# Performance work log

Measured on AMD Instinct MI355X. Metric: run time of the kernel, lower is better.

## Reference

```python
import jax, jax.numpy as jnp
import numpy as np

B, L, D, OUT, EXP = 4, 4096, 128, 55, 2
D2 = 2 * D

def _ln(x, g, b):
    m = jnp.mean(x, axis=-1, keepdims=True)
    v = jnp.mean((x - m) ** 2, axis=-1, keepdims=True)
    return (x - m) / jnp.sqrt(v + 1e-5) * g + b

def setup_inputs() -> dict:
    key = jax.random.key(0)
    ks = iter(jax.random.split(key, 32))
    w = lambda shape: jax.random.normal(next(ks), shape, jnp.float32) * 0.02
    inp = {
        'x1': jax.random.normal(next(ks), (B, L, D), jnp.float32),
        'x2': jax.random.normal(next(ks), (B, L, D), jnp.float32),
        'ln1_g': jnp.ones((D,)), 'ln1_b': jnp.zeros((D,)),
        'ln2_g': jnp.ones((D,)), 'ln2_b': jnp.zeros((D,)),
        'Wq': w((D, D)), 'bq': jnp.zeros((D,)),
        'Wv1': w((D, D)), 'bv1': jnp.zeros((D,)),
        'Wk': w((D, D)), 'bk': jnp.zeros((D,)),
        'Wv2': w((D, D)), 'bv2': jnp.zeros((D,)),
        'Wp1': w((D, D)), 'bp1': jnp.zeros((D,)),
        'Wp2': w((D, D)), 'bp2': jnp.zeros((D,)),
        'lnf_g': jnp.ones((D2,)), 'lnf_b': jnp.zeros((D2,)),
        'Wf1': w((D2, EXP * D2)), 'bf1': jnp.zeros((EXP * D2,)),
        'Wf2': w((EXP * D2, D2)), 'bf2': jnp.zeros((D2,)),
        'ln3_g': jnp.ones((D2,)), 'ln3_b': jnp.zeros((D2,)),
        'Wo': w((D2, OUT)), 'bo': jnp.zeros((OUT,)),
    }
    return inp

def reference(x1, x2, ln1_g, ln1_b, ln2_g, ln2_b, Wq, bq, Wv1, bv1, Wk, bk,
              Wv2, bv2, Wp1, bp1, Wp2, bp2, lnf_g, lnf_b, Wf1, bf1, Wf2, bf2,
              ln3_g, ln3_b, Wo, bo):
    res1, res2 = x1, x2
    x1n = _ln(x1, ln1_g, ln1_b)
    x2n = _ln(x2, ln2_g, ln2_b)
    q1 = x1n @ Wq + bq        # [B,L,D]
    v1 = x1n @ Wv1 + bv1
    k2 = x2n @ Wk + bk
    v2 = x2n @ Wv2 + bv2
    # faithful to torch: energy = einsum('bqd,bkd->bqk', keys2, queries1)
    energy = jnp.einsum('bqd,bkd->bqk', k2, q1)
    att = jax.nn.softmax(energy / jnp.sqrt(jnp.float32(D)), axis=-1)  # [B,L,L]
    out1 = jnp.einsum('bal,blv->bav', att, v1) @ Wp1 + bp1
    out2 = jnp.einsum('bal,blv->bav', att, v2) @ Wp2 + bp2
    y1 = out1 + res1
    y2 = out2 + res2
    x = jnp.concatenate([y1, y2], axis=-1)  # [B,L,2D]
    res = x
    h = _ln(x, lnf_g, lnf_b)
    h = jax.nn.gelu(h @ Wf1 + bf1, approximate=False) @ Wf2 + bf2
    x = _ln(h + res, ln3_g, ln3_b)
    return x @ Wo + bo  # [B,L,OUT]
```

## Files before the change

### kernel.cpp

```cpp
#include <hip/hip_runtime.h>
#include <hip/hip_fp16.h>

typedef _Float16 half8 __attribute__((ext_vector_type(8)));
typedef _Float16 half4 __attribute__((ext_vector_type(4)));
typedef float f32x4 __attribute__((ext_vector_type(4)));
typedef float f32x16 __attribute__((ext_vector_type(16)));
typedef int  i32x8 __attribute__((ext_vector_type(8)));
typedef long lng2 __attribute__((ext_vector_type(2)));

#define B_   4
#define L_   4096
#define D_   128
#define M_   (B_*L_)
#define D2_  256
#define H_   512
#define OUT_ 55

__device__ __forceinline__ f32x4 mfma16(half8 a, half8 b, f32x4 c) {
    return __builtin_amdgcn_mfma_f32_16x16x32_f16(a, b, c, 0, 0, 0);
}
__device__ __forceinline__ f32x16 mfma_mx32(i32x8 a, i32x8 b, f32x16 c) {
    return __builtin_amdgcn_mfma_scale_f32_32x32x64_f8f6f4(a, b, c, 0, 0, 0, 127, 0, 127);
}
__device__ __forceinline__ int pk4(float a, float b, float c, float d) {
    int t = __builtin_amdgcn_cvt_pk_fp8_f32(a, b, 0, false);
    return __builtin_amdgcn_cvt_pk_fp8_f32(c, d, t, true);
}
__device__ __forceinline__ float fexp2(float x) { return __builtin_amdgcn_exp2f(x); }

#define KSCL (0.08838834764831845f * 1.4426950408889634f)

#define WQ_OFF   0
#define WV1_OFF  16384
#define WK_OFF   32768
#define WV2_OFF  49152
#define WP1_OFF  65536
#define WP2_OFF  81920
#define WF1_OFF  98304
#define WF2_OFF  229376
#define WO_OFF   360448


__global__ void prep_kernel(const float* Wq, const float* Wv1, const float* Wk,
                            const float* Wv2, const float* Wp1, const float* Wp2,
                            const float* Wf1, const float* Wf2, const float* Wo,
                            _Float16* wsw, float* rowsum) {
    int id = blockIdx.y;
    int t  = blockIdx.x * 256 + threadIdx.x;
    if (id == 9) {
        if (t < 4096) ((f32x4*)rowsum)[t] = f32x4{0.f, 0.f, 0.f, 0.f};
        return;
    }
    const float* src = nullptr; int K = 0, N = 0, Npad = 0, off = 0;
    switch (id) {
        case 0: src = Wq;  K = 128; N = 128; Npad = 128; off = WQ_OFF;  break;
        case 1: src = Wv1; K = 128; N = 128; Npad = 128; off = WV1_OFF; break;
        case 2: src = Wk;  K = 128; N = 128; Npad = 128; off = WK_OFF;  break;
        case 3: src = Wv2; K = 128; N = 128; Npad = 128; off = WV2_OFF; break;
        case 4: src = Wp1; K = 128; N = 128; Npad = 128; off = WP1_OFF; break;
        case 5: src = Wp2; K = 128; N = 128; Npad = 128; off = WP2_OFF; break;
        case 6: src = Wf1; K = 256; N = 512; Npad = 512; off = WF1_OFF; break;
        case 7: src = Wf2; K = 512; N = 256; Npad = 256; off = WF2_OFF; break;
        case 8: src = Wo;  K = 256; N = 55;  Npad = 64;  off = WO_OFF;  break;
        default: return;
    }
    int total = K * Npad;
    if (t >= total) return;
    int k = t / Npad, n = t % Npad;
    float v = (n < N) ? src[k * N + n] : 0.f;
    int s = k >> 5, c = n >> 4, ln = n & 15;
    int q, j;
    if (id == 4 || id == 5) { q = (k >> 2) & 3; j = (k & 3) + (((k >> 4) & 1) << 2); }
    else                    { q = (k >> 3) & 3; j = k & 7; }
    int nc = Npad >> 4;
    wsw[off + ((size_t)((s * nc + c) * 64 + q * 16 + ln)) * 8 + j] = (_Float16)v;
}


__global__ __launch_bounds__(256) void proj_kernel(const float* x1, const float* x2,
        const _Float16* wsw,
        const float* ln1_g, const float* ln1_b, const float* ln2_g, const float* ln2_b,
        const float* bq, const float* bv1, const float* bk, const float* bv2,
        _Float16* q1, _Float16* k2, unsigned char* vsw8) {
    int g2 = blockIdx.y;
    const float* X  = g2 ? x2 : x1;
    const float* lg = g2 ? ln2_g : ln1_g;
    const float* lb = g2 ? ln2_b : ln1_b;
    int wave = threadIdx.x >> 6, lane = threadIdx.x & 63;
    int quad = lane >> 4, ln = lane & 15;
    int mbase = blockIdx.x * 64 + wave * 16;
    int lt = mbase >> 4;

    const float* xr = X + (size_t)(mbase + ln) * D_;
    float xv[4][8];
    float sum = 0.f, sq = 0.f;
    #pragma unroll
    for (int s = 0; s < 4; s++) {
        f32x4 v0 = *(const f32x4*)(xr + s * 32 + quad * 8);
        f32x4 v1 = *(const f32x4*)(xr + s * 32 + quad * 8 + 4);
        #pragma unroll
        for (int j = 0; j < 4; j++) {
            xv[s][j]     = v0[j];
            xv[s][j + 4] = v1[j];
            sum += v0[j] + v1[j];
            sq  += v0[j] * v0[j] + v1[j] * v1[j];
        }
    }
    sum += __shfl_xor(sum, 16); sum += __shfl_xor(sum, 32);
    sq  += __shfl_xor(sq, 16);  sq  += __shfl_xor(sq, 32);
    float mean = sum * (1.f / 128.f);
    float var  = sq * (1.f / 128.f) - mean * mean;
    float inv  = rsqrtf(var + 1e-5f);
    half8 a[4];
    #pragma unroll
    for (int s = 0; s < 4; s++) {
        f32x4 g0 = *(const f32x4*)(lg + s * 32 + quad * 8);
        f32x4 g1 = *(const f32x4*)(lg + s * 32 + quad * 8 + 4);
        f32x4 b0 = *(const f32x4*)(lb + s * 32 + quad * 8);
        f32x4 b1 = *(const f32x4*)(lb + s * 32 + quad * 8 + 4);
        #pragma unroll
        for (int j = 0; j < 4; j++) {
            a[s][j]     = (_Float16)((xv[s][j] - mean) * inv * g0[j] + b0[j]);
            a[s][j + 4] = (_Float16)((xv[s][j + 4] - mean) * inv * g1[j] + b1[j]);
        }
    }

    {
        const _Float16* Bw = wsw + (g2 ? WK_OFF : WQ_OFF);
        const float* bias = g2 ? bk : bq;
        float scl = g2 ? KSCL : 1.f;
        _Float16* out = g2 ? k2 : q1;
        f32x4 acc[8];
        #pragma unroll
        for (int c = 0; c < 8; c++) acc[c] = f32x4{0.f, 0.f, 0.f, 0.f};
        half8 Wc[4], Wn[4];
        #pragma unroll
        for (int s = 0; s < 4; s++)
            Wc[s] = *(const half8*)(Bw + ((size_t)((s * 8 + 0) * 64 + lane)) * 8);
        #pragma unroll
        for (int c = 0; c < 8; c++) {
            int cn = (c < 7) ? c + 1 : 7;
            #pragma unroll
            for (int s = 0; s < 4; s++)
                Wn[s] = *(const half8*)(Bw + ((size_t)((s * 8 + cn) * 64 + lane)) * 8);
            #pragma unroll
            for (int s = 0; s < 4; s++)
                acc[c] = mfma16(a[s], Wc[s], acc[c]);
            #pragma unroll
            for (int s = 0; s < 4; s++) Wc[s] = Wn[s];
        }
        #pragma unroll
        for (int c = 0; c < 8; c++) {
            int n = c * 16 + ln;
            float bv = bias[n];
            #pragma unroll
            for (int r = 0; r < 4; r++) {
                int s_o = c >> 1, q_o = ((c & 1) << 1) | (ln >> 3), j = ln & 7;
                out[((size_t)((lt * 4 + s_o) * 64 + q_o * 16 + (quad * 4 + r))) * 8 + j]
                    = (_Float16)((acc[c][r] + bv) * scl);
            }
        }
    }

    {
        const _Float16* Bw = wsw + (g2 ? WV2_OFF : WV1_OFF);
        const float* bias = g2 ? bv2 : bv1;
        int cbase = g2 ? 8 : 0;
        f32x4 acc[8];
        #pragma unroll
        for (int c = 0; c < 8; c++) acc[c] = f32x4{0.f, 0.f, 0.f, 0.f};
        half8 Wc[4], Wn[4];
        #pragma unroll
        for (int s = 0; s < 4; s++)
            Wc[s] = *(const half8*)(Bw + ((size_t)((s * 8 + 0) * 64 + lane)) * 8);
        #pragma unroll
        for (int c = 0; c < 8; c++) {
            int cn = (c < 7) ? c + 1 : 7;
            #pragma unroll
            for (int s = 0; s < 4; s++)
                Wn[s] = *(const half8*)(Bw + ((size_t)((s * 8 + cn) * 64 + lane)) * 8);
            #pragma unroll
            for (int s = 0; s < 4; s++)
                acc[c] = mfma16(a[s], Wc[s], acc[c]);
            #pragma unroll
            for (int s = 0; s < 4; s++) Wc[s] = Wn[s];
        }
        int b = mbase >> 12;
        int k64 = (mbase & (L_ - 1)) >> 6;
        int gg = quad >> 1, jh = quad & 1;
        unsigned char* Vb = vsw8 + (size_t)b * (1u << 20);
        #pragma unroll
        for (int c = 0; c < 8; c++) {
            int n = c * 16 + ln;
            float bv = bias[n];
            int pk = pk4(acc[c][0] + bv, acc[c][1] + bv, acc[c][2] + bv, acc[c][3] + bv);
            int v32 = (cbase + c) >> 1;
            int lane32 = ((c & 1) << 4) + ln + 32 * gg;
            *(int*)(Vb + ((size_t)((k64 * 8 + v32) * 64 + lane32)) * 32 + 16 * jh + 4 * wave) = pk;
        }
    }
}

__global__ __launch_bounds__(256) void score_kernel(
        const _Float16* __restrict__ q1sw, const _Float16* __restrict__ k2sw,
        unsigned char* __restrict__ pmat8, float* __restrict__ rowsum) {
    int w = threadIdx.x >> 6, lane = threadIdx.x & 63;
    int quad = lane >> 4, ln = lane & 15;
    int b = blockIdx.z;
    int kL0 = blockIdx.y * 128 + (w & 1) * 64;
    int mL0 = blockIdx.x * 128 + (w >> 1) * 64;
    int ltk = ((b << 12) + kL0) >> 4;
    int ltm = ((b << 12) + mL0) >> 4;

    f32x4 acc[4][4];
    #pragma unroll
    for (int i = 0; i < 4; i++)
        #pragma unroll
        for (int j = 0; j < 4; j++) acc[i][j] = f32x4{0.f, 0.f, 0.f, 0.f};

    #pragma unroll
    for (int s = 0; s < 4; s++) {
        half8 a[4], bq[4];
        #pragma unroll
        for (int i = 0; i < 4; i++)
            a[i] = *(const half8*)(q1sw + ((size_t)(((ltk + i) * 4 + s) * 64 + lane)) * 8);
        #pragma unroll
        for (int j = 0; j < 4; j++)
            bq[j] = *(const half8*)(k2sw + ((size_t)(((ltm + j) * 4 + s) * 64 + lane)) * 8);
        #pragma unroll
        for (int i = 0; i < 4; i++)
            #pragma unroll
            for (int j = 0; j < 4; j++)
                acc[i][j] = mfma16(a[i], bq[j], acc[i][j]);
    }

    unsigned char* Pb = pmat8 + (size_t)b * (16u << 20);
    int k64 = kL0 >> 6;
    int gg = quad >> 1, jh = quad & 1;
    #pragma unroll
    for (int j = 0; j < 4; j++) {
        int4 d;
        float csum = 0.f;
        #pragma unroll
        for (int i = 0; i < 4; i++) {
            float p0 = fexp2(acc[i][j][0]);
            float p1 = fexp2(acc[i][j][1]);
            float p2 = fexp2(acc[i][j][2]);
            float p3 = fexp2(acc[i][j][3]);
            csum += (p0 + p1) + (p2 + p3);
            ((int*)&d)[i] = pk4(p0, p1, p2, p3);
        }
        csum += __shfl_xor(csum, 16);
        csum += __shfl_xor(csum, 32);
        if (lane < 16)
            atomicAdd(&rowsum[(b << 12) + mL0 + j * 16 + ln], csum);
        int att32 = (mL0 >> 5) + (j >> 1);
        int a32 = ((j & 1) << 4) + ln;
        *(int4*)(Pb + ((size_t)((att32 * 64 + k64) * 64 + a32 + 32 * gg)) * 32 + 16 * jh) = d;
    }
}

__global__ __launch_bounds__(512) void pv_kernel(
        const unsigned char* __restrict__ pmat8, const unsigned char* __restrict__ vsw8,
        const float* __restrict__ rowsum,
        _Float16* __restrict__ att1, _Float16* __restrict__ att2) {
    __shared__ f32x4 part[4][2][4][64];
    int w = threadIdx.x >> 6, lane = threadIdx.x & 63;
    int wc = w & 3, kh = w >> 2;
    int rowG0 = blockIdx.x * 32;
    int b = rowG0 >> 12;
    int att32 = (rowG0 & (L_ - 1)) >> 5;
    const unsigned char* Pb = pmat8 + (size_t)b * (16u << 20);
    const unsigned char* Vb = vsw8 + (size_t)b * (1u << 20);

    const unsigned char* Vbase = Vb + (size_t)(wc * 2) * 2048 + (size_t)lane * 32;
    const unsigned char* Pbase = Pb + (size_t)att32 * 131072 + (size_t)lane * 32;
    int sp0 = kh * 32;

    f32x16 acc0, acc1;
    #pragma unroll
    for (int i = 0; i < 16; i++) { acc0[i] = 0.f; acc1[i] = 0.f; }

    #define PVLOAD(dA, dB, dP, sp) do {                                       \
        dA = *(const i32x8*)(Vbase + (size_t)(sp) * 16384);                   \
        dB = *(const i32x8*)(Vbase + (size_t)(sp) * 16384 + 2048);            \
        dP = *(const i32x8*)(Pbase + (size_t)(sp) * 2048);                    \
    } while (0)

    i32x8 a0, b0, p0, a1, b1, p1, na, nb, np;
    PVLOAD(a0, b0, p0, sp0);
    PVLOAD(a1, b1, p1, sp0 + 1);
    for (int ii = 0; ii < 32; ii += 2) {
        int s2 = sp0 + ((ii + 2 < 32) ? ii + 2 : 31);
        int s3 = sp0 + ((ii + 3 < 32) ? ii + 3 : 31);
        PVLOAD(na, nb, np, s2);
        acc0 = mfma_mx32(a0, p0, acc0);
        acc1 = mfma_mx32(b0, p0, acc1);
        a0 = na; b0 = nb; p0 = np;
        PVLOAD(na, nb, np, s3);
        acc0 = mfma_mx32(a1, p1, acc0);
        acc1 = mfma_mx32(b1, p1, acc1);
        a1 = na; b1 = nb; p1 = np;
    }
    #undef PVLOAD

    if (kh == 1) {
        #pragma unroll
        for (int q = 0; q < 4; q++) {
            part[wc][0][q][lane] = f32x4{acc0[q * 4 + 0], acc0[q * 4 + 1],
                                         acc0[q * 4 + 2], acc0[q * 4 + 3]};
            part[wc][1][q][lane] = f32x4{acc1[q * 4 + 0], acc1[q * 4 + 1],
                                         acc1[q * 4 + 2], acc1[q * 4 + 3]};
        }
    }
    __syncthreads();
    if (kh == 0) {
        int aglob = rowG0 + (lane & 31);
        float inv = 1.f / rowsum[aglob];
        int g = lane >> 5;
        int lt = aglob >> 4, lnr = lane & 15;
        #pragma unroll
        for (int t = 0; t < 2; t++) {
            int v32 = wc * 2 + t;
            _Float16* att = (v32 >= 4) ? att2 : att1;
            int s = v32 & 3;
            #pragma unroll
            for (int q = 0; q < 4; q++) {
                f32x4 pp = part[wc][t][q][lane];
                half4 hv;
                #pragma unroll
                for (int rr = 0; rr < 4; rr++) {
                    float v = ((t == 0) ? acc0[q * 4 + rr] : acc1[q * 4 + rr]) + pp[rr];
                    hv[rr] = (_Float16)(v * inv);
                }
                *(half4*)(att + ((size_t)((lt * 4 + s) * 64 + q * 16 + lnr)) * 8 + 4 * g) = hv;
            }
        }
    }
}

__global__ __launch_bounds__(256) void attn_out_kernel(const _Float16* att1, const _Float16* att2,
        const _Float16* wsw, const float* bp1, const float* bp2,
        const float* x1, const float* x2, const float* lnf_g, const float* lnf_b,
        _Float16* res, _Float16* xn) {
    __shared__ float sst[2][16][2][2];
    int w = threadIdx.x >> 6, lane = threadIdx.x & 63;
    int quad = lane >> 4, ln = lane & 15;
    int rt = w & 1, st = w >> 1;
    int mbase = blockIdx.x * 32 + rt * 16;
    int lt = mbase >> 4;
    const _Float16* att = st ? att2 : att1;
    const _Float16* Wp = wsw + (st ? WP2_OFF : WP1_OFF);
    const float* bp = st ? bp2 : bp1;
    const float* xres = st ? x2 : x1;

    half8 a[4];
    #pragma unroll
    for (int s = 0; s < 4; s++)
        a[s] = *(const half8*)(att + ((size_t)((lt * 4 + s) * 64 + lane)) * 8);

    f32x4 y[8];
    #pragma unroll
    for (int c = 0; c < 8; c++) y[c] = f32x4{0,0,0,0};

    half8 Wc[4], Wn[4];
    #pragma unroll
    for (int s = 0; s < 4; s++)
        Wc[s] = *(const half8*)(Wp + ((size_t)((s * 8 + 0) * 64 + lane)) * 8);
    #pragma unroll
    for (int c = 0; c < 8; c++) {
        int cn = (c < 7) ? c + 1 : 7;
        #pragma unroll
        for (int s = 0; s < 4; s++)
            Wn[s] = *(const half8*)(Wp + ((size_t)((s * 8 + cn) * 64 + lane)) * 8);
        #pragma unroll
        for (int s = 0; s < 4; s++)
            y[c] = mfma16(a[s], Wc[s], y[c]);
        #pragma unroll
        for (int s = 0; s < 4; s++) Wc[s] = Wn[s];
    }

    float psum[4] = {0,0,0,0}, psq[4] = {0,0,0,0};
    #pragma unroll
    for (int c = 0; c < 8; c++) {
        int n = c * 16 + ln;
        float bv = bp[n];
        #pragma unroll
        for (int r = 0; r < 4; r++) {
            int m = mbase + quad * 4 + r;
            float v = y[c][r] + bv + xres[(size_t)m * D_ + n];
            y[c][r] = v; psum[r] += v; psq[r] += v * v;
        }
    }
    #pragma unroll
    for (int off = 1; off < 16; off <<= 1)
        #pragma unroll
        for (int r = 0; r < 4; r++) { psum[r] += __shfl_xor(psum[r], off); psq[r] += __shfl_xor(psq[r], off); }
    if (ln == 0)
        #pragma unroll
        for (int r = 0; r < 4; r++) {
            sst[rt][quad * 4 + r][st][0] = psum[r];
            sst[rt][quad * 4 + r][st][1] = psq[r];
        }
    __syncthreads();
    #pragma unroll
    for (int r = 0; r < 4; r++) {
        float su = sst[rt][quad * 4 + r][0][0] + sst[rt][quad * 4 + r][1][0];
        float sq = sst[rt][quad * 4 + r][0][1] + sst[rt][quad * 4 + r][1][1];
        float mean = su * (1.f / 256.f);
        float var = sq * (1.f / 256.f) - mean * mean;
        float inv = rsqrtf(var + 1e-5f);
        int m = mbase + quad * 4 + r;
        int lt_m = m >> 4;
        #pragma unroll
        for (int c = 0; c < 8; c++) {
            int colg = st * 128 + c * 16 + ln;
            res[(size_t)m * D2_ + colg] = (_Float16)y[c][r];
            float yn = (y[c][r] - mean) * inv * lnf_g[colg] + lnf_b[colg];
            int s_x = colg >> 5, q_x = (colg >> 3) & 3, j = colg & 7;
            xn[((size_t)((lt_m * 8 + s_x) * 64 + q_x * 16 + (m & 15))) * 8 + j] = (_Float16)yn;
        }
    }
}

__global__ __launch_bounds__(256) void ffn1_kernel(const _Float16* xn, const _Float16* wsw,
        const float* bf1, _Float16* h) {
    int wave = threadIdx.x >> 6, lane = threadIdx.x & 63;
    int quad = lane >> 4, ln = lane & 15;
    int mbase = blockIdx.x * 64 + wave * 16;
    int lt = mbase >> 4;
    int nt = blockIdx.y;
    const _Float16* W = wsw + WF1_OFF;

    half8 a[8];
    #pragma unroll
    for (int s = 0; s < 8; s++)
        a[s] = *(const half8*)(xn + ((size_t)((lt * 8 + s) * 64 + lane)) * 8);

    f32x4 acc[8];
    #pragma unroll
    for (int c = 0; c < 8; c++) acc[c] = f32x4{0,0,0,0};

    half8 Wc[8], Wn[8];
    #pragma unroll
    for (int s = 0; s < 8; s++)
        Wc[s] = *(const half8*)(W + ((size_t)((s * 32 + nt * 8) * 64 + lane)) * 8);
    #pragma unroll
    for (int c = 0; c < 8; c++) {
        int cn = (c < 7) ? c + 1 : 7;
        #pragma unroll
        for (int s = 0; s < 8; s++)
            Wn[s] = *(const half8*)(W + ((size_t)((s * 32 + nt * 8 + cn) * 64 + lane)) * 8);
        #pragma unroll
        for (int s = 0; s < 8; s++)
            acc[c] = mfma16(a[s], Wc[s], acc[c]);
        #pragma unroll
        for (int s = 0; s < 8; s++) Wc[s] = Wn[s];
    }
    #pragma unroll
    for (int c = 0; c < 8; c++) {
        int n = nt * 128 + c * 16 + ln;
        float bv = bf1[n];
        int s_h = n >> 5, q_h = (n >> 3) & 3, j = n & 7;
        #pragma unroll
        for (int r = 0; r < 4; r++) {
            float v = acc[c][r] + bv;
            float u = 0.7978845608f * (v + 0.044715f * v * v * v);
            float e = fexp2(-2.8853900818f * u);
            float ge = v * __builtin_amdgcn_rcpf(1.f + e);
            h[((size_t)((lt * 16 + s_h) * 64 + q_h * 16 + (quad * 4 + r))) * 8 + j] = (_Float16)ge;
        }
    }
}

__global__ __launch_bounds__(256) void ffn2_out_kernel(const _Float16* h, const _Float16* wsw,
        const float* bf2, const _Float16* res, const float* g3, const float* b3,
        const float* bo, float* out) {
    __shared__ float sst[2][16][2][2];
    __shared__ _Float16 xt[8192];
    __shared__ f32x4 pc[2][4][64];
    int w = threadIdx.x >> 6, lane = threadIdx.x & 63;
    int quad = lane >> 4, ln = lane & 15;
    int rt = w & 1, nh = w >> 1;
    int mb = blockIdx.x * 32 + rt * 16;
    int lt = mb >> 4;
    const _Float16* W = wsw + WF2_OFF;

    f32x4 acc[8];
    #pragma unroll
    for (int c = 0; c < 8; c++) acc[c] = f32x4{0,0,0,0};

    half8 aC, aN;
    half8 Wc[8], Wn[8];
    aC = *(const half8*)(h + ((size_t)((lt * 16 + 0) * 64 + lane)) * 8);
    #pragma unroll
    for (int c = 0; c < 8; c++)
        Wc[c] = *(const half8*)(W + ((size_t)((0 * 16 + nh * 8 + c) * 64 + lane)) * 8);

    #pragma unroll
    for (int s = 0; s < 16; s++) {
        int sn = (s < 15) ? s + 1 : 15;
        aN = *(const half8*)(h + ((size_t)((lt * 16 + sn) * 64 + lane)) * 8);
        #pragma unroll
        for (int c = 0; c < 8; c++)
            Wn[c] = *(const half8*)(W + ((size_t)((sn * 16 + nh * 8 + c) * 64 + lane)) * 8);
        #pragma unroll
        for (int c = 0; c < 8; c++)
            acc[c] = mfma16(aC, Wc[c], acc[c]);
        aC = aN;
        #pragma unroll
        for (int c = 0; c < 8; c++) Wc[c] = Wn[c];
    }

    float y[8][4];
    float psum[4] = {0,0,0,0}, psq[4] = {0,0,0,0};
    #pragma unroll
    for (int c = 0; c < 8; c++) {
        int n = nh * 128 + c * 16 + ln;
        float bv = bf2[n];
        #pragma unroll
        for (int r = 0; r < 4; r++) {
            int m = mb + quad * 4 + r;
            float v = acc[c][r] + bv + (float)res[(size_t)m * D2_ + n];
            y[c][r] = v; psum[r] += v; psq[r] += v * v;
        }
    }
    #pragma unroll
    for (int off = 1; off < 16; off <<= 1)
        #pragma unroll
        for (int r = 0; r < 4; r++) { psum[r] += __shfl_xor(psum[r], off); psq[r] += __shfl_xor(psq[r], off); }
    if (ln == 0)
        #pragma unroll
        for (int r = 0; r < 4; r++) { sst[rt][quad * 4 + r][nh][0] = psum[r]; sst[rt][quad * 4 + r][nh][1] = psq[r]; }
    __syncthreads();
    #pragma unroll
    for (int r = 0; r < 4; r++) {
        float su = sst[rt][quad * 4 + r][0][0] + sst[rt][quad * 4 + r][1][0];
        float sq = sst[rt][quad * 4 + r][0][1] + sst[rt][quad * 4 + r][1][1];
        float mean = su * (1.f / 256.f);
        float var = sq * (1.f / 256.f) - mean * mean;
        float invs = rsqrtf(var + 1e-5f);
        #pragma unroll
        for (int c = 0; c < 8; c++) {
            int n = nh * 128 + c * 16 + ln;
            float yn = (y[c][r] - mean) * invs * g3[n] + b3[n];
            int s_x = n >> 5, q_x = (n >> 3) & 3, j = n & 7;
            xt[((rt * 8 + s_x) * 64 + q_x * 16 + (quad * 4 + r)) * 8 + j] = (_Float16)yn;
        }
    }
    __syncthreads();

    int rt2 = w & 1, kh = w >> 1;
    const _Float16* Wo = wsw + WO_OFF;
    f32x4 oacc[4];
    #pragma unroll
    for (int c = 0; c < 4; c++) oacc[c] = f32x4{0,0,0,0};
    #pragma unroll
    for (int ss = 0; ss < 4; ss++) {
        int s = kh * 4 + ss;
        half8 a = *(const half8*)(xt + ((size_t)((rt2 * 8 + s) * 64 + lane)) * 8);
        #pragma unroll
        for (int c = 0; c < 4; c++)
            oacc[c] = mfma16(a, *(const half8*)(Wo + ((size_t)((s * 4 + c) * 64 + lane)) * 8), oacc[c]);
    }
    if (kh == 1)
        #pragma unroll
        for (int c = 0; c < 4; c++) pc[rt2][c][lane] = oacc[c];
    __syncthreads();
    if (kh == 0) {
        int mb2 = blockIdx.x * 32 + rt2 * 16;
        #pragma unroll
        for (int c = 0; c < 4; c++) {
            f32x4 p = pc[rt2][c][lane];
            int n = c * 16 + ln;
            if (n < OUT_) {
                float bv = bo[n];
                #pragma unroll
                for (int r = 0; r < 4; r++)
                    out[(size_t)(mb2 + quad * 4 + r) * OUT_ + n] = oacc[c][r] + p[r] + bv;
            }
        }
    }
}

extern "C" void kernel_launch(void* const* d_in, const int* in_sizes, int n_in,
                              void* d_out, int out_size, void* d_ws, size_t ws_size,
                              hipStream_t stream) {
    const float* x1    = (const float*)d_in[0];
    const float* x2    = (const float*)d_in[1];
    const float* ln1_g = (const float*)d_in[2];
    const float* ln1_b = (const float*)d_in[3];
    const float* ln2_g = (const float*)d_in[4];
    const float* ln2_b = (const float*)d_in[5];
    const float* Wq    = (const float*)d_in[6];
    const float* bq    = (const float*)d_in[7];
    const float* Wv1   = (const float*)d_in[8];
    const float* bv1   = (const float*)d_in[9];
    const float* Wk    = (const float*)d_in[10];
    const float* bk    = (const float*)d_in[11];
    const float* Wv2   = (const float*)d_in[12];
    const float* bv2   = (const float*)d_in[13];
    const float* Wp1   = (const float*)d_in[14];
    const float* bp1   = (const float*)d_in[15];
    const float* Wp2   = (const float*)d_in[16];
    const float* bp2   = (const float*)d_in[17];
    const float* lnf_g = (const float*)d_in[18];
    const float* lnf_b = (const float*)d_in[19];
    const float* Wf1   = (const float*)d_in[20];
    const float* bf1   = (const float*)d_in[21];
    const float* Wf2   = (const float*)d_in[22];
    const float* bf2   = (const float*)d_in[23];
    const float* ln3_g = (const float*)d_in[24];
    const float* ln3_b = (const float*)d_in[25];
    const float* Wo    = (const float*)d_in[26];
    const float* bo    = (const float*)d_in[27];
    float* out = (float*)d_out;

    char* ws = (char*)d_ws;
    const size_t MB = 1 << 20;
    _Float16* q1sw   = (_Float16*)(ws + 0 * MB);
    _Float16* k2sw   = (_Float16*)(ws + 4 * MB);
    unsigned char* vsw8 = (unsigned char*)(ws + 8 * MB);
    _Float16* att1   = (_Float16*)(ws + 12 * MB);
    _Float16* att2   = (_Float16*)(ws + 16 * MB);
    _Float16* wsw    = (_Float16*)(ws + 28 * MB);
    float*    rowsum = (float*)   (ws + 29 * MB);
    _Float16* res    = (_Float16*)(ws + 30 * MB);
    _Float16* xn     = (_Float16*)(ws + 46 * MB);
    _Float16* h      = (_Float16*)(ws + 54 * MB);
    unsigned char* pmat8 = (unsigned char*)(ws + 78 * MB);

    prep_kernel<<<dim3(512, 10), 256, 0, stream>>>(Wq, Wv1, Wk, Wv2, Wp1, Wp2, Wf1, Wf2, Wo,
                                                   wsw, rowsum);
    proj_kernel<<<dim3(M_ / 64, 2), 256, 0, stream>>>(x1, x2, wsw,
                                                      ln1_g, ln1_b, ln2_g, ln2_b,
                                                      bq, bv1, bk, bv2,
                                                      q1sw, k2sw, vsw8);
    score_kernel<<<dim3(32, 32, 4), 256, 0, stream>>>(q1sw, k2sw, pmat8, rowsum);
    pv_kernel<<<dim3(M_ / 32), 512, 0, stream>>>(pmat8, vsw8, rowsum, att1, att2);
    attn_out_kernel<<<dim3(M_ / 32), 256, 0, stream>>>(att1, att2, wsw, bp1, bp2,
                                                       x1, x2, lnf_g, lnf_b, res, xn);
    ffn1_kernel<<<dim3(M_ / 64, 4), 256, 0, stream>>>(xn, wsw, bf1, h);
    ffn2_out_kernel<<<dim3(M_ / 32), 256, 0, stream>>>(h, wsw, bf2, res, ln3_g, ln3_b, bo, out);
}
```

Measured before the change: 236.0 us.

## Retile PV kernel so each block covers 128 rows and half the V columns

Each block of the P·V kernel now handles 128 attention rows, with one 32-row group per wave pair, and one of two V halves selected by blockIdx.y, instead of 32 rows across all V columns. Each wave loads one P tile and reuses it across four V sub-tiles, and V tiles are shared by the four row-group waves through cache. This is meant to cut redundant loads of the large FP8 probability matrix, since each P element is now read twice per batch instead of four times. In exchange each wave holds twice as many accumulator and prefetch registers, which may lower occupancy, and LDS use doubles.

```diff
diff --git a/kernel.cpp b/kernel.cpp
--- a/kernel.cpp
+++ b/kernel.cpp
@@ -264,78 +264,90 @@
         const unsigned char* __restrict__ pmat8, const unsigned char* __restrict__ vsw8,
         const float* __restrict__ rowsum,
         _Float16* __restrict__ att1, _Float16* __restrict__ att2) {
-    __shared__ f32x4 part[4][2][4][64];
+    __shared__ f32x4 part[4][4][4][64];
     int w = threadIdx.x >> 6, lane = threadIdx.x & 63;
-    int wc = w & 3, kh = w >> 2;
-    int rowG0 = blockIdx.x * 32;
+    int a = w & 3, kh = w >> 2;
+    int vh = blockIdx.y;
+    int rowG0 = blockIdx.x * 128;
     int b = rowG0 >> 12;
-    int att32 = (rowG0 & (L_ - 1)) >> 5;
+    int att32 = ((rowG0 & (L_ - 1)) >> 5) + a;
     const unsigned char* Pb = pmat8 + (size_t)b * (16u << 20);
     const unsigned char* Vb = vsw8 + (size_t)b * (1u << 20);
 
-    const unsigned char* Vbase = Vb + (size_t)(wc * 2) * 2048 + (size_t)lane * 32;
+    const unsigned char* Vbase = Vb + (size_t)(vh * 4) * 2048 + (size_t)lane * 32;
     const unsigned char* Pbase = Pb + (size_t)att32 * 131072 + (size_t)lane * 32;
     int sp0 = kh * 32;
 
-    f32x16 acc0, acc1;
-    #pragma unroll
-    for (int i = 0; i < 16; i++) { acc0[i] = 0.f; acc1[i] = 0.f; }
-
-    #define PVLOAD(dA, dB, dP, sp) do {                                       \
-        dA = *(const i32x8*)(Vbase + (size_t)(sp) * 16384);                   \
-        dB = *(const i32x8*)(Vbase + (size_t)(sp) * 16384 + 2048);            \
-        dP = *(const i32x8*)(Pbase + (size_t)(sp) * 2048);                    \
+    f32x16 acc0, acc1, acc2, acc3;
+    #pragma unroll
+    for (int i = 0; i < 16; i++) { acc0[i] = 0.f; acc1[i] = 0.f; acc2[i] = 0.f; acc3[i] = 0.f; }
+
+    #define PVLOAD(d0, d1, d2, d3, dp, sp) do {                               \
+        const unsigned char* vp_ = Vbase + (size_t)(sp) * 16384;              \
+        d0 = *(const i32x8*)(vp_);                                            \
+        d1 = *(const i32x8*)(vp_ + 2048);                                     \
+        d2 = *(const i32x8*)(vp_ + 4096);                                     \
+        d3 = *(const i32x8*)(vp_ + 6144);                                     \
+        dp = *(const i32x8*)(Pbase + (size_t)(sp) * 2048);                    \
     } while (0)
 
-    i32x8 a0, b0, p0, a1, b1, p1, na, nb, np;
-    PVLOAD(a0, b0, p0, sp0);
-    PVLOAD(a1, b1, p1, sp0 + 1);
+    i32x8 v00, v01, v02, v03, p0, v10, v11, v12, v13, p1, n0, n1, n2, n3, np;
+    PVLOAD(v00, v01, v02, v03, p0, sp0);
+    PVLOAD(v10, v11, v12, v13, p1, sp0 + 1);
     for (int ii = 0; ii < 32; ii += 2) {
-        int s2 = sp0 + ((ii + 2 < 32) ? ii + 2 : 31);
+        int s2 = sp0 + ((ii + 2 < 32) ? ii + 2 : 30);
         int s3 = sp0 + ((ii + 3 < 32) ? ii + 3 : 31);
-        PVLOAD(na, nb, np, s2);
-        acc0 = mfma_mx32(a0, p0, acc0);
-        acc1 = mfma_mx32(b0, p0, acc1);
-        a0 = na; b0 = nb; p0 = np;
-        PVLOAD(na, nb, np, s3);
-        acc0 = mfma_mx32(a1, p1, acc0);
-        acc1 = mfma_mx32(b1, p1, acc1);
-        a1 = na; b1 = nb; p1 = np;
+        PVLOAD(n0, n1, n2, n3, np, s2);
+        acc0 = mfma_mx32(v00, p0, acc0);
+        acc1 = mfma_mx32(v01, p0, acc1);
+        acc2 = mfma_mx32(v02, p0, acc2);
+        acc3 = mfma_mx32(v03, p0, acc3);
+        v00 = n0; v01 = n1; v02 = n2; v03 = n3; p0 = np;
+        PVLOAD(n0, n1, n2, n3, np, s3);
+        acc0 = mfma_mx32(v10, p1, acc0);
+        acc1 = mfma_mx32(v11, p1, acc1);
+        acc2 = mfma_mx32(v12, p1, acc2);
+        acc3 = mfma_mx32(v13, p1, acc3);
+        v10 = n0; v11 = n1; v12 = n2; v13 = n3; p1 = np;
     }
     #undef PVLOAD
 
     if (kh == 1) {
         #pragma unroll
         for (int q = 0; q < 4; q++) {
-            part[wc][0][q][lane] = f32x4{acc0[q * 4 + 0], acc0[q * 4 + 1],
-                                         acc0[q * 4 + 2], acc0[q * 4 + 3]};
-            part[wc][1][q][lane] = f32x4{acc1[q * 4 + 0], acc1[q * 4 + 1],
-                                         acc1[q * 4 + 2], acc1[q * 4 + 3]};
+            part[a][0][q][lane] = f32x4{acc0[q * 4 + 0], acc0[q * 4 + 1],
+                                        acc0[q * 4 + 2], acc0[q * 4 + 3]};
+            part[a][1][q][lane] = f32x4{acc1[q * 4 + 0], acc1[q * 4 + 1],
+                                        acc1[q * 4 + 2], acc1[q * 4 + 3]};
+            part[a][2][q][lane] = f32x4{acc2[q * 4 + 0], acc2[q * 4 + 1],
+                                        acc2[q * 4 + 2], acc2[q * 4 + 3]};
+            part[a][3][q][lane] = f32x4{acc3[q * 4 + 0], acc3[q * 4 + 1],
+                                        acc3[q * 4 + 2], acc3[q * 4 + 3]};
         }
     }
     __syncthreads();
     if (kh == 0) {
-        int aglob = rowG0 + (lane & 31);
+        int aglob = rowG0 + a * 32 + (lane & 31);
         float inv = 1.f / rowsum[aglob];
         int g = lane >> 5;
         int lt = aglob >> 4, lnr = lane & 15;
-        #pragma unroll
-        for (int t = 0; t < 2; t++) {
-            int v32 = wc * 2 + t;
-            _Float16* att = (v32 >= 4) ? att2 : att1;
-            int s = v32 & 3;
-            #pragma unroll
-            for (int q = 0; q < 4; q++) {
-                f32x4 pp = part[wc][t][q][lane];
-                half4 hv;
-                #pragma unroll
-                for (int rr = 0; rr < 4; rr++) {
-                    float v = ((t == 0) ? acc0[q * 4 + rr] : acc1[q * 4 + rr]) + pp[rr];
-                    hv[rr] = (_Float16)(v * inv);
-                }
-                *(half4*)(att + ((size_t)((lt * 4 + s) * 64 + q * 16 + lnr)) * 8 + 4 * g) = hv;
-            }
-        }
+        _Float16* att = vh ? att2 : att1;
+        #define PVSTORE(accT, t) do {                                         \
+            _Pragma("unroll")                                                 \
+            for (int q = 0; q < 4; q++) {                                     \
+                f32x4 pp = part[a][t][q][lane];                               \
+                half4 hv;                                                     \
+                _Pragma("unroll")                                             \
+                for (int rr = 0; rr < 4; rr++)                                \
+                    hv[rr] = (_Float16)((accT[q * 4 + rr] + pp[rr]) * inv);   \
+                *(half4*)(att + ((size_t)((lt * 4 + (t)) * 64 + q * 16 + lnr)) * 8 + 4 * g) = hv; \
+            }                                                                 \
+        } while (0)
+        PVSTORE(acc0, 0);
+        PVSTORE(acc1, 1);
+        PVSTORE(acc2, 2);
+        PVSTORE(acc3, 3);
+        #undef PVSTORE
     }
 }
 
@@ -637,7 +649,7 @@
                                                       bq, bv1, bk, bv2,
                                                       q1sw, k2sw, vsw8);
     score_kernel<<<dim3(32, 32, 4), 256, 0, stream>>>(q1sw, k2sw, pmat8, rowsum);
-    pv_kernel<<<dim3(M_ / 32), 512, 0, stream>>>(pmat8, vsw8, rowsum, att1, att2);
+    pv_kernel<<<dim3(M_ / 128, 2), 512, 0, stream>>>(pmat8, vsw8, rowsum, att1, att2);
     attn_out_kernel<<<dim3(M_ / 32), 256, 0, stream>>>(att1, att2, wsw, bp1, bp2,
                                                        x1, x2, lnf_g, lnf_b, res, xn);
     ffn1_kernel<<<dim3(M_ / 64, 4), 256, 0, stream>>>(xn, wsw, bf1, h);
```

Result: slower. 245.8 us (+4.1%).

## Switch PV stage to 16x16x128 FP8 MFMA and drop LDS split-K reduction

Applied to the files above, without the earlier changes.

The P·V kernel moves from the 32x32x64 scaled FP8 MFMA with a two-way split over the key dimension to the 16x16x128 variant. Each wave now covers a 16-row tile across the full key range, so the shared-memory partial sums and the __syncthreads reduction go away. The P and V producers in the score and projection kernels are relaid out to match the new operand format, and launch bounds request 4 blocks per CU. The trade-off is that each wave runs a longer serial key loop, P loads are repeated across the V-column waves, and the smaller MFMA shape does less work per operand load.

```diff
diff --git a/kernel.cpp b/kernel.cpp
--- a/kernel.cpp
+++ b/kernel.cpp
@@ -4,9 +4,7 @@
 typedef _Float16 half8 __attribute__((ext_vector_type(8)));
 typedef _Float16 half4 __attribute__((ext_vector_type(4)));
 typedef float f32x4 __attribute__((ext_vector_type(4)));
-typedef float f32x16 __attribute__((ext_vector_type(16)));
 typedef int  i32x8 __attribute__((ext_vector_type(8)));
-typedef long lng2 __attribute__((ext_vector_type(2)));
 
 #define B_   4
 #define L_   4096
@@ -19,8 +17,8 @@
 __device__ __forceinline__ f32x4 mfma16(half8 a, half8 b, f32x4 c) {
     return __builtin_amdgcn_mfma_f32_16x16x32_f16(a, b, c, 0, 0, 0);
 }
-__device__ __forceinline__ f32x16 mfma_mx32(i32x8 a, i32x8 b, f32x16 c) {
-    return __builtin_amdgcn_mfma_scale_f32_32x32x64_f8f6f4(a, b, c, 0, 0, 0, 127, 0, 127);
+__device__ __forceinline__ f32x4 mfma_mx16(i32x8 a, i32x8 b, f32x4 c) {
+    return __builtin_amdgcn_mfma_scale_f32_16x16x128_f8f6f4(a, b, c, 0, 0, 0, 127, 0, 127);
 }
 __device__ __forceinline__ int pk4(float a, float b, float c, float d) {
     int t = __builtin_amdgcn_cvt_pk_fp8_f32(a, b, 0, false);
@@ -165,7 +163,6 @@
     {
         const _Float16* Bw = wsw + (g2 ? WV2_OFF : WV1_OFF);
         const float* bias = g2 ? bv2 : bv1;
-        int cbase = g2 ? 8 : 0;
         f32x4 acc[8];
         #pragma unroll
         for (int c = 0; c < 8; c++) acc[c] = f32x4{0.f, 0.f, 0.f, 0.f};
@@ -186,17 +183,17 @@
             for (int s = 0; s < 4; s++) Wc[s] = Wn[s];
         }
         int b = mbase >> 12;
-        int k64 = (mbase & (L_ - 1)) >> 6;
-        int gg = quad >> 1, jh = quad & 1;
+        int k128 = (mbase & (L_ - 1)) >> 7;
+        int h = (mbase >> 6) & 1;
         unsigned char* Vb = vsw8 + (size_t)b * (1u << 20);
         #pragma unroll
         for (int c = 0; c < 8; c++) {
             int n = c * 16 + ln;
             float bv = bias[n];
             int pk = pk4(acc[c][0] + bv, acc[c][1] + bv, acc[c][2] + bv, acc[c][3] + bv);
-            int v32 = (cbase + c) >> 1;
-            int lane32 = ((c & 1) << 4) + ln + 32 * gg;
-            *(int*)(Vb + ((size_t)((k64 * 8 + v32) * 64 + lane32)) * 32 + 16 * jh + 4 * wave) = pk;
+            int v16 = g2 * 8 + c;
+            *(int*)(Vb + ((size_t)((k128 * 16 + v16) * 64 + quad * 16 + ln)) * 32
+                       + 16 * h + 4 * wave) = pk;
         }
     }
 }
@@ -235,8 +232,8 @@
     }
 
     unsigned char* Pb = pmat8 + (size_t)b * (16u << 20);
-    int k64 = kL0 >> 6;
-    int gg = quad >> 1, jh = quad & 1;
+    int k128 = kL0 >> 7;
+    int kh = (kL0 >> 6) & 1;
     #pragma unroll
     for (int j = 0; j < 4; j++) {
         int4 d;
@@ -254,88 +251,74 @@
         csum += __shfl_xor(csum, 32);
         if (lane < 16)
             atomicAdd(&rowsum[(b << 12) + mL0 + j * 16 + ln], csum);
-        int att32 = (mL0 >> 5) + (j >> 1);
-        int a32 = ((j & 1) << 4) + ln;
-        *(int4*)(Pb + ((size_t)((att32 * 64 + k64) * 64 + a32 + 32 * gg)) * 32 + 16 * jh) = d;
-    }
-}
-
-__global__ __launch_bounds__(512) void pv_kernel(
+        int att16 = (mL0 >> 4) + j;
+        *(int4*)(Pb + ((size_t)((att16 * 32 + k128) * 64 + quad * 16 + ln)) * 32
+                    + 16 * kh) = d;
+    }
+}
+
+__global__ __launch_bounds__(512, 4) void pv_kernel(
         const unsigned char* __restrict__ pmat8, const unsigned char* __restrict__ vsw8,
         const float* __restrict__ rowsum,
         _Float16* __restrict__ att1, _Float16* __restrict__ att2) {
-    __shared__ f32x4 part[4][2][4][64];
     int w = threadIdx.x >> 6, lane = threadIdx.x & 63;
-    int wc = w & 3, kh = w >> 2;
+    int rt = w & 1, vq = w >> 1;
     int rowG0 = blockIdx.x * 32;
     int b = rowG0 >> 12;
-    int att32 = (rowG0 & (L_ - 1)) >> 5;
+    int att16 = ((rowG0 & (L_ - 1)) >> 4) + rt;
     const unsigned char* Pb = pmat8 + (size_t)b * (16u << 20);
     const unsigned char* Vb = vsw8 + (size_t)b * (1u << 20);
-
-    const unsigned char* Vbase = Vb + (size_t)(wc * 2) * 2048 + (size_t)lane * 32;
-    const unsigned char* Pbase = Pb + (size_t)att32 * 131072 + (size_t)lane * 32;
-    int sp0 = kh * 32;
-
-    f32x16 acc0, acc1;
-    #pragma unroll
-    for (int i = 0; i < 16; i++) { acc0[i] = 0.f; acc1[i] = 0.f; }
-
-    #define PVLOAD(dA, dB, dP, sp) do {                                       \
-        dA = *(const i32x8*)(Vbase + (size_t)(sp) * 16384);                   \
-        dB = *(const i32x8*)(Vbase + (size_t)(sp) * 16384 + 2048);            \
-        dP = *(const i32x8*)(Pbase + (size_t)(sp) * 2048);                    \
+    const unsigned char* Pbase = Pb + (size_t)att16 * 65536 + (size_t)lane * 32;
+    const unsigned char* Vbase = Vb + (size_t)(vq * 4) * 2048 + (size_t)lane * 32;
+
+    f32x4 acc[4];
+    #pragma unroll
+    for (int i = 0; i < 4; i++) acc[i] = f32x4{0.f, 0.f, 0.f, 0.f};
+
+    #define VLOAD(vv, sp) do {                                                \
+        const unsigned char* vp_ = Vbase + (size_t)(sp) * 32768;              \
+        vv[0] = *(const i32x8*)(vp_);                                         \
+        vv[1] = *(const i32x8*)(vp_ + 2048);                                  \
+        vv[2] = *(const i32x8*)(vp_ + 4096);                                  \
+        vv[3] = *(const i32x8*)(vp_ + 6144);                                  \
     } while (0)
-
-    i32x8 a0, b0, p0, a1, b1, p1, na, nb, np;
-    PVLOAD(a0, b0, p0, sp0);
-    PVLOAD(a1, b1, p1, sp0 + 1);
-    for (int ii = 0; ii < 32; ii += 2) {
-        int s2 = sp0 + ((ii + 2 < 32) ? ii + 2 : 31);
-        int s3 = sp0 + ((ii + 3 < 32) ? ii + 3 : 31);
-        PVLOAD(na, nb, np, s2);
-        acc0 = mfma_mx32(a0, p0, acc0);
-        acc1 = mfma_mx32(b0, p0, acc1);
-        a0 = na; b0 = nb; p0 = np;
-        PVLOAD(na, nb, np, s3);
-        acc0 = mfma_mx32(a1, p1, acc0);
-        acc1 = mfma_mx32(b1, p1, acc1);
-        a1 = na; b1 = nb; p1 = np;
-    }
-    #undef PVLOAD
-
-    if (kh == 1) {
-        #pragma unroll
-        for (int q = 0; q < 4; q++) {
-            part[wc][0][q][lane] = f32x4{acc0[q * 4 + 0], acc0[q * 4 + 1],
-                                         acc0[q * 4 + 2], acc0[q * 4 + 3]};
-            part[wc][1][q][lane] = f32x4{acc1[q * 4 + 0], acc1[q * 4 + 1],
-                                         acc1[q * 4 + 2], acc1[q * 4 + 3]};
-        }
-    }
-    __syncthreads();
-    if (kh == 0) {
-        int aglob = rowG0 + (lane & 31);
-        float inv = 1.f / rowsum[aglob];
-        int g = lane >> 5;
-        int lt = aglob >> 4, lnr = lane & 15;
-        #pragma unroll
-        for (int t = 0; t < 2; t++) {
-            int v32 = wc * 2 + t;
-            _Float16* att = (v32 >= 4) ? att2 : att1;
-            int s = v32 & 3;
-            #pragma unroll
-            for (int q = 0; q < 4; q++) {
-                f32x4 pp = part[wc][t][q][lane];
-                half4 hv;
-                #pragma unroll
-                for (int rr = 0; rr < 4; rr++) {
-                    float v = ((t == 0) ? acc0[q * 4 + rr] : acc1[q * 4 + rr]) + pp[rr];
-                    hv[rr] = (_Float16)(v * inv);
-                }
-                *(half4*)(att + ((size_t)((lt * 4 + s) * 64 + q * 16 + lnr)) * 8 + 4 * g) = hv;
-            }
-        }
+    #define PLOAD(pp, sp) do {                                                \
+        pp = *(const i32x8*)(Pbase + (size_t)(sp) * 2048);                    \
+    } while (0)
+
+    i32x8 v0[4], nv[4], p0, p1, np;
+    VLOAD(v0, 0);
+    PLOAD(p0, 0);
+    PLOAD(p1, 1);
+    for (int ii = 0; ii < 32; ii++) {
+        int sv = (ii + 1 < 32) ? ii + 1 : 31;
+        int sp = (ii + 2 < 32) ? ii + 2 : 31;
+        VLOAD(nv, sv);
+        PLOAD(np, sp);
+        acc[0] = mfma_mx16(v0[0], p0, acc[0]);
+        acc[1] = mfma_mx16(v0[1], p0, acc[1]);
+        acc[2] = mfma_mx16(v0[2], p0, acc[2]);
+        acc[3] = mfma_mx16(v0[3], p0, acc[3]);
+        v0[0] = nv[0]; v0[1] = nv[1]; v0[2] = nv[2]; v0[3] = nv[3];
+        p0 = p1; p1 = np;
+    }
+    #undef VLOAD
+    #undef PLOAD
+
+    int m = rowG0 + rt * 16 + (lane & 15);
+    float inv = 1.f / rowsum[m];
+    int gq = lane >> 4;
+    int lt = m >> 4, lnr = lane & 15;
+    #pragma unroll
+    for (int i = 0; i < 4; i++) {
+        int v16g = vq * 4 + i;
+        _Float16* att = (v16g >= 8) ? att2 : att1;
+        int n = (v16g * 16 + gq * 4) & 127;
+        int s = n >> 5, q = (n >> 3) & 3, jb = n & 7;
+        half4 hv;
+        #pragma unroll
+        for (int rr = 0; rr < 4; rr++) hv[rr] = (_Float16)(acc[i][rr] * inv);
+        *(half4*)(att + ((size_t)((lt * 4 + s) * 64 + q * 16 + lnr)) * 8 + jb) = hv;
     }
 }
 
```

Result: slower. 252.3 us (+6.9%).
